# Kernel tuning notes

Hardware: AMD Instinct MI355X
Metric: run time of the kernel (lower is better)

Reference implementation:

```python
import jax, jax.numpy as jnp
import numpy as np

EMBED_DIM = 1024
NUM_HEADS = 16
HEAD_DIM = EMBED_DIM // NUM_HEADS
SCALE = HEAD_DIM ** (-0.5)


def setup_inputs() -> dict:
    key = jax.random.key(0)
    ks = jax.random.split(key, 13)
    B, N, D = 4, 4096, EMBED_DIM
    lin_scale = 1.0 / np.sqrt(D)
    inp = {
        "q": jax.random.normal(ks[0], (B, N, D), dtype=jnp.float32),
        "k": jax.random.normal(ks[1], (B, N, D), dtype=jnp.float32),
        "v": jax.random.normal(ks[2], (B, N, D), dtype=jnp.float32),
        "Wq": jax.random.uniform(ks[3], (D, D), jnp.float32, -lin_scale, lin_scale),
        "bq": jax.random.uniform(ks[4], (D,), jnp.float32, -lin_scale, lin_scale),
        "Wk": jax.random.uniform(ks[5], (D, D), jnp.float32, -lin_scale, lin_scale),
        "bk": jax.random.uniform(ks[6], (D,), jnp.float32, -lin_scale, lin_scale),
        "Wv": jax.random.uniform(ks[7], (D, D), jnp.float32, -lin_scale, lin_scale),
        "bv": jax.random.uniform(ks[8], (D,), jnp.float32, -lin_scale, lin_scale),
        "q_alpha": jax.random.normal(ks[9], (NUM_HEADS, HEAD_DIM), dtype=jnp.float32),
        "k_beta": jax.random.normal(ks[10], (NUM_HEADS, HEAD_DIM), dtype=jnp.float32),
        "Wo": jax.random.uniform(ks[11], (D, D), jnp.float32, -lin_scale, lin_scale),
        "bo": jax.random.uniform(ks[12], (D,), jnp.float32, -lin_scale, lin_scale),
    }
    return inp


def reference(q, k, v, Wq, bq, Wk, bk, Wv, bv, q_alpha, k_beta, Wo, bo):
    B, N, D = q.shape
    H, Dh = NUM_HEADS, HEAD_DIM
    # torch Linear: x @ W.T + b
    Q = (q @ Wq.T + bq).reshape(B, N, H, Dh)
    K = (k @ Wk.T + bk).reshape(B, N, H, Dh)
    V = (v @ Wv.T + bv).reshape(B, N, H, Dh)
    # alpha: [B,N,H] -> softmax over N
    alpha = jnp.einsum('bnhd,hd->bnh', Q, q_alpha) * SCALE
    alpha = jax.nn.softmax(alpha, axis=1)
    # global_q: [B,1,H,Dh]
    global_q = jnp.einsum('bnhd,bnh->bhd', Q, alpha)[:, None]
    P = K * global_q  # [B,N,H,Dh]
    beta = jnp.einsum('bnhd,hd->bnh', P, k_beta) * SCALE
    beta = jax.nn.softmax(beta, axis=1)
    global_v = jnp.einsum('bnhd,bnh->bhd', V, beta)[:, None]
    out = (Q + global_v).reshape(B, N, D)
    out = out @ Wo.T + bo
    return out
```

## Files before the change

### kernel.cpp

```cpp
#include <hip/hip_runtime.h>
#include <hip/hip_bf16.h>
#include <cstdint>
#include <cstddef>

#define SEQ    4096
#define NB     4
#define DIM    1024
#define NHEAD  16
#define HDIM   64
#define MROWS  (NB * SEQ)
#define SCALEF 0.125f
#define NT     16

typedef short          s16x8 __attribute__((ext_vector_type(8)));
typedef unsigned short u16x8 __attribute__((ext_vector_type(8)));
typedef float          f32x4 __attribute__((ext_vector_type(4)));
typedef unsigned short u16;

__device__ __forceinline__ u16 f2bf(float f) {
  return __builtin_bit_cast(u16, __float2bfloat16(f));
}
__device__ __forceinline__ float bf2f(u16 u) {
  return __builtin_bit_cast(float, (uint32_t)u << 16);
}
__device__ __forceinline__ void gload_lds16(const void* g, void* l) {
  __builtin_amdgcn_global_load_lds(
      (const __attribute__((address_space(1))) void*)g,
      (__attribute__((address_space(3))) void*)l, 16, 0, 0);
}

__global__ __launch_bounds__(256) void cvt_weights(
    const float* __restrict__ w0, const float* __restrict__ w1,
    const float* __restrict__ w2, const float* __restrict__ w3,
    u16* __restrict__ o0, u16* __restrict__ o1,
    u16* __restrict__ o2, u16* __restrict__ o3)
{
  int t = blockIdx.x * 256 + threadIdx.x;
  int m = t >> 17;
  int off = (t & 131071) * 8;
  const float* s = (m == 0) ? w0 : (m == 1) ? w1 : (m == 2) ? w2 : w3;
  u16*         d = (m == 0) ? o0 : (m == 1) ? o1 : (m == 2) ? o2 : o3;
  float4 a = ((const float4*)(s + off))[0];
  float4 b = ((const float4*)(s + off))[1];
  u16x8 p;
  p[0] = f2bf(a.x); p[1] = f2bf(a.y); p[2] = f2bf(a.z); p[3] = f2bf(a.w);
  p[4] = f2bf(b.x); p[5] = f2bf(b.y); p[6] = f2bf(b.z); p[7] = f2bf(b.w);
  *(u16x8*)(d + off) = p;
}

__global__ __launch_bounds__(256) void cvt_act(
    const float* __restrict__ s, u16* __restrict__ d)
{
  int t = blockIdx.x * 256 + threadIdx.x;
  int off = t * 8;
  float4 a = ((const float4*)(s + off))[0];
  float4 b = ((const float4*)(s + off))[1];
  u16x8 p;
  p[0] = f2bf(a.x); p[1] = f2bf(a.y); p[2] = f2bf(a.z); p[3] = f2bf(a.w);
  p[4] = f2bf(b.x); p[5] = f2bf(b.y); p[6] = f2bf(b.z); p[7] = f2bf(b.w);
  *(u16x8*)(d + off) = p;
}

template<int MODE>
__global__ __launch_bounds__(512) void gemm256(
    const u16* __restrict__ A, const u16* __restrict__ W,
    const float* __restrict__ bias, u16* __restrict__ Cb, float* __restrict__ Cf,
    const float* __restrict__ c2, int do_alpha,
    const float* __restrict__ qalpha, float* __restrict__ la)
{
  extern __shared__ __align__(16) char smem[];
  const int tid = threadIdx.x;
  const int lane = tid & 63, wave = tid >> 6;
  const int wr = wave >> 2, wc = wave & 3;
  const int fr = lane & 15, fq = lane >> 4;
  const int m0 = blockIdx.x * 256, n0 = blockIdx.y * 256;
  const int wrow = wr * 128, wcol = wc * 64;

  const int arow = tid >> 3;
  const int scol = (((tid & 7) ^ ((tid >> 3) & 7)) * 8);

  f32x4 acc[8][4];
  #pragma unroll
  for (int i = 0; i < 8; ++i)
    #pragma unroll
    for (int j = 0; j < 4; ++j) acc[i][j] = (f32x4){0.f, 0.f, 0.f, 0.f};

  auto stA = [&](int kt, int h) {
    const u16* g = A + (size_t)(m0 + h * 128) * DIM + kt * 64;
    char* l = smem + (kt & 1) * 32768 + h * 16384;
    gload_lds16(g + (size_t)arow * DIM + scol,        l + tid * 16);
    gload_lds16(g + (size_t)(64 + arow) * DIM + scol, l + 8192 + tid * 16);
  };
  auto stB = [&](int kt, int h) {
    const u16* g = W + (size_t)(n0 + h * 128) * DIM + kt * 64;
    char* l = smem + 65536 + (kt & 1) * 32768 + h * 16384;
    gload_lds16(g + (size_t)arow * DIM + scol,        l + tid * 16);
    gload_lds16(g + (size_t)(64 + arow) * DIM + scol, l + 8192 + tid * 16);
  };
  auto ldsoff = [&](int R, int ks) -> size_t {
    return (size_t)R * 128 + (size_t)((ks * 64 + fq * 16) ^ ((R & 7) << 4));
  };

  stA(0, 0); stA(0, 1); stB(0, 0); stB(0, 1);
  stA(1, 0);
  asm volatile("s_waitcnt vmcnt(2)" ::: "memory");
  asm volatile("s_barrier" ::: "memory");

  for (int t = 0; t < NT; ++t) {
    const char* Abase = smem + (t & 1) * 32768;
    const char* Bbase = smem + 65536 + (t & 1) * 32768;
    s16x8 areg[4][2];
    #pragma unroll
    for (int p = 0; p < 4; ++p) {
      const int mq = p >> 1, nq = p & 1;
      s16x8 breg[2][2];
      #pragma unroll
      for (int j = 0; j < 2; ++j)
        #pragma unroll
        for (int ks = 0; ks < 2; ++ks)
          breg[j][ks] = *(const s16x8*)(Bbase + ldsoff(wcol + (nq * 2 + j) * 16 + fr, ks));
      if (nq == 0) {
        #pragma unroll
        for (int i = 0; i < 4; ++i)
          #pragma unroll
          for (int ks = 0; ks < 2; ++ks)
            areg[i][ks] = *(const s16x8*)(Abase + ldsoff(wrow + (mq * 4 + i) * 16 + fr, ks));
      }
      if (p == 0 && t + 1 < NT) stA(t + 1, 1);
      if (p == 1 && t + 1 < NT) stB(t + 1, 0);
      if (p == 2 && t + 1 < NT) stB(t + 1, 1);
      if (p == 3 && t + 2 < NT) stA(t + 2, 0);

      asm volatile("s_barrier" ::: "memory");
      __builtin_amdgcn_s_setprio(1);
      #pragma unroll
      for (int i = 0; i < 4; ++i)
        #pragma unroll
        for (int j = 0; j < 2; ++j)
          #pragma unroll
          for (int ks = 0; ks < 2; ++ks)
            acc[mq * 4 + i][nq * 2 + j] = __builtin_amdgcn_mfma_f32_16x16x32_bf16(
                areg[i][ks], breg[j][ks], acc[mq * 4 + i][nq * 2 + j], 0, 0, 0);
      __builtin_amdgcn_s_setprio(0);
      if (p < 3) {
        asm volatile("s_barrier" ::: "memory");
      } else {
        if (t == NT - 2) asm volatile("s_waitcnt vmcnt(0)" ::: "memory");
        else             asm volatile("s_waitcnt vmcnt(2)" ::: "memory");
        asm volatile("s_barrier" ::: "memory");
      }
    }
  }

  if constexpr (MODE == 0) {
    #pragma unroll
    for (int ni = 0; ni < 4; ++ni) {
      const int col = n0 + wcol + ni * 16 + fr;
      const float bvv = bias[col];
      #pragma unroll
      for (int mi = 0; mi < 8; ++mi)
        #pragma unroll
        for (int r = 0; r < 4; ++r)
          acc[mi][ni][r] += bvv;
    }
    #pragma unroll
    for (int ni = 0; ni < 4; ++ni) {
      const int col = n0 + wcol + ni * 16 + fr;
      #pragma unroll
      for (int mi = 0; mi < 8; ++mi) {
        #pragma unroll
        for (int r = 0; r < 4; ++r) {
          const int row = m0 + wrow + mi * 16 + fq * 4 + r;
          Cb[(size_t)row * DIM + col] = f2bf(acc[mi][ni][r]);
        }
      }
    }
    if (do_alpha) {
      const int h = (n0 >> 6) + wc;
      float qa0 = qalpha[h * HDIM + 0 * 16 + fr];
      float qa1 = qalpha[h * HDIM + 1 * 16 + fr];
      float qa2 = qalpha[h * HDIM + 2 * 16 + fr];
      float qa3 = qalpha[h * HDIM + 3 * 16 + fr];
      #pragma unroll
      for (int mi = 0; mi < 8; ++mi) {
        #pragma unroll
        for (int r = 0; r < 4; ++r) {
          float p = acc[mi][0][r] * qa0 + acc[mi][1][r] * qa1
                  + acc[mi][2][r] * qa2 + acc[mi][3][r] * qa3;
          p += __shfl_xor(p, 1);
          p += __shfl_xor(p, 2);
          p += __shfl_xor(p, 4);
          p += __shfl_xor(p, 8);
          if (fr == 0) {
            const int row = m0 + wrow + mi * 16 + fq * 4 + r;
            la[((size_t)(row >> 12) * NHEAD + h) * SEQ + (row & (SEQ - 1))] = p * SCALEF;
          }
        }
      }
    }
  } else {
    const int bidx = m0 >> 12;
    #pragma unroll
    for (int ni = 0; ni < 4; ++ni) {
      const int col = n0 + wcol + ni * 16 + fr;
      const float cv = c2[bidx * DIM + col];
      #pragma unroll
      for (int mi = 0; mi < 8; ++mi) {
        #pragma unroll
        for (int r = 0; r < 4; ++r) {
          const int row = m0 + wrow + mi * 16 + fq * 4 + r;
          Cf[(size_t)row * DIM + col] = acc[mi][ni][r] + cv;
        }
      }
    }
  }
}

__global__ __launch_bounds__(256) void softmax_norm(
    float* __restrict__ l, float* __restrict__ zbuf)
{
  const int bh = blockIdx.x;
  const int tid = threadIdx.x, lane = tid & 63, wave = tid >> 6;
  float* p = l + (size_t)bh * SEQ;
  __shared__ float red[8];

  float4 v[4];
  #pragma unroll
  for (int i = 0; i < 4; ++i) v[i] = ((const float4*)p)[i * 256 + tid];

  float m = -1e30f;
  #pragma unroll
  for (int i = 0; i < 4; ++i)
    m = fmaxf(m, fmaxf(fmaxf(v[i].x, v[i].y), fmaxf(v[i].z, v[i].w)));
  #pragma unroll
  for (int o = 32; o; o >>= 1) m = fmaxf(m, __shfl_xor(m, o));
  if (lane == 0) red[wave] = m;
  __syncthreads();
  m = fmaxf(fmaxf(red[0], red[1]), fmaxf(red[2], red[3]));

  float s = 0.f;
  #pragma unroll
  for (int i = 0; i < 4; ++i) {
    v[i].x = __expf(v[i].x - m); v[i].y = __expf(v[i].y - m);
    v[i].z = __expf(v[i].z - m); v[i].w = __expf(v[i].w - m);
    s += (v[i].x + v[i].y) + (v[i].z + v[i].w);
  }
  #pragma unroll
  for (int o = 32; o; o >>= 1) s += __shfl_xor(s, o);
  if (lane == 0) red[4 + wave] = s;
  __syncthreads();
  s = (red[4] + red[5]) + (red[6] + red[7]);

  float inv = 1.0f / s;
  #pragma unroll
  for (int i = 0; i < 4; ++i) {
    v[i].x *= inv; v[i].y *= inv; v[i].z *= inv; v[i].w *= inv;
    ((float4*)p)[i * 256 + tid] = v[i];
  }
  if (tid < HDIM) zbuf[bh * HDIM + tid] = 0.f;
}

__global__ __launch_bounds__(256) void accum_weighted(
    const u16* __restrict__ X, const float* __restrict__ w,
    float* __restrict__ outp)
{
  const int bh = blockIdx.y, chunk = blockIdx.x;
  const int b = bh >> 4, h = bh & 15;
  const int tid = threadIdx.x, lane = tid & 63, wave = tid >> 6;
  const int rsub = lane >> 3, cl = lane & 7;
  const size_t base = (size_t)b * SEQ * DIM + h * HDIM;
  const int n0 = chunk * 512;

  float acc[8] = {0, 0, 0, 0, 0, 0, 0, 0};
  for (int it = 0; it < 16; ++it) {
    int n = n0 + it * 32 + wave * 8 + rsub;
    u16x8 u = *(const u16x8*)(X + base + (size_t)n * DIM + cl * 8);
    float wv = w[(size_t)bh * SEQ + n];
    #pragma unroll
    for (int j = 0; j < 8; ++j) acc[j] += wv * bf2f(u[j]);
  }
  #pragma unroll
  for (int j = 0; j < 8; ++j) {
    acc[j] += __shfl_xor(acc[j], 8);
    acc[j] += __shfl_xor(acc[j], 16);
    acc[j] += __shfl_xor(acc[j], 32);
  }
  __shared__ float part[4][64];
  if (rsub == 0) {
    #pragma unroll
    for (int j = 0; j < 8; ++j) part[wave][cl * 8 + j] = acc[j];
  }
  __syncthreads();
  if (tid < HDIM) {
    float s = (part[0][tid] + part[1][tid]) + (part[2][tid] + part[3][tid]);
    atomicAdd(&outp[bh * HDIM + tid], s);
  }
}

__global__ __launch_bounds__(256) void make_vecb(
    const float* __restrict__ gq, const float* __restrict__ kbeta,
    float* __restrict__ vecb)
{
  int t = blockIdx.x * 256 + threadIdx.x;
  int h = (t >> 6) & 15, d = t & 63;
  vecb[t] = gq[t] * kbeta[h * HDIM + d] * SCALEF;
}

__global__ __launch_bounds__(256) void logits_beta(
    const u16* __restrict__ Kb, const float* __restrict__ vecb,
    float* __restrict__ lb)
{
  __shared__ float vb[NHEAD][HDIM];
  const int rg = blockIdx.x;
  const int b = rg >> 8;
  const int tid = threadIdx.x, lane = tid & 63, wave = tid >> 6;

  for (int i = tid; i < NHEAD * HDIM; i += 256)
    ((float*)vb)[i] = vecb[b * DIM + i];
  __syncthreads();

  const int h = lane >> 2, dq = (lane & 3) * 16;
  #pragma unroll
  for (int i = 0; i < 4; ++i) {
    int gr = rg * 16 + wave * 4 + i;
    const u16* rp = Kb + (size_t)gr * DIM + h * HDIM + dq;
    u16x8 u0 = *(const u16x8*)rp;
    u16x8 u1 = *(const u16x8*)(rp + 8);
    float dot = 0.f;
    #pragma unroll
    for (int j = 0; j < 8; ++j) dot += bf2f(u0[j]) * vb[h][dq + j];
    #pragma unroll
    for (int j = 0; j < 8; ++j) dot += bf2f(u1[j]) * vb[h][dq + 8 + j];
    dot += __shfl_xor(dot, 1);
    dot += __shfl_xor(dot, 2);
    if ((lane & 3) == 0) {
      lb[((size_t)b * NHEAD + h) * SEQ + (gr & (SEQ - 1))] = dot;
    }
  }
}

__global__ __launch_bounds__(256) void gv_wo_kernel(
    const float* __restrict__ gv, const float* __restrict__ Wo,
    const float* __restrict__ bo, float* __restrict__ c2)
{
  int wid = blockIdx.x * 4 + (threadIdx.x >> 6);
  int b = wid >> 10, j = wid & 1023;
  int lane = threadIdx.x & 63;
  float acc = 0.f;
  #pragma unroll
  for (int c = 0; c < 16; ++c) {
    int kk = c * 64 + lane;
    acc += gv[b * DIM + kk] * Wo[(size_t)j * DIM + kk];
  }
  #pragma unroll
  for (int o = 32; o; o >>= 1) acc += __shfl_down(acc, o);
  if (lane == 0) c2[wid] = acc + bo[j];
}

extern "C" void kernel_launch(void* const* d_in, const int* in_sizes, int n_in,
                              void* d_out, int out_size, void* d_ws, size_t ws_size,
                              hipStream_t stream) {
  const float* q  = (const float*)d_in[0];
  const float* k  = (const float*)d_in[1];
  const float* v  = (const float*)d_in[2];
  const float* Wq = (const float*)d_in[3];
  const float* bq = (const float*)d_in[4];
  const float* Wk = (const float*)d_in[5];
  const float* bk = (const float*)d_in[6];
  const float* Wv = (const float*)d_in[7];
  const float* bv = (const float*)d_in[8];
  const float* qa = (const float*)d_in[9];
  const float* kb = (const float*)d_in[10];
  const float* Wo = (const float*)d_in[11];
  const float* bo = (const float*)d_in[12];
  float* out = (float*)d_out;

  u16* Qb  = (u16*)d_ws;
  u16* Kb  = Qb + (size_t)MROWS * DIM;
  u16* Vb  = Kb + (size_t)MROWS * DIM;
  u16* Wqb = Vb + (size_t)MROWS * DIM;
  u16* Wkb = Wqb + (size_t)DIM * DIM;
  u16* Wvb = Wkb + (size_t)DIM * DIM;
  u16* Wob = Wvb + (size_t)DIM * DIM;
  float* la   = (float*)(Wob + (size_t)DIM * DIM);
  float* lb   = la + (size_t)NB * NHEAD * SEQ;
  float* gq   = lb + (size_t)NB * NHEAD * SEQ;
  float* gv   = gq + NB * DIM;
  float* vecb = gv + NB * DIM;
  float* c2   = vecb + NB * DIM;

  u16* actb = (u16*)d_out;

  const dim3 g256(MROWS / 256, DIM / 256);
  const size_t ldsb = 131072;

  cvt_weights<<<2048, 256, 0, stream>>>(Wq, Wk, Wv, Wo, Wqb, Wkb, Wvb, Wob);

  cvt_act<<<8192, 256, 0, stream>>>(q, actb);
  gemm256<0><<<g256, 512, ldsb, stream>>>(actb, Wqb, bq, Qb, nullptr, nullptr, 1, qa, la);
  cvt_act<<<8192, 256, 0, stream>>>(k, actb);
  gemm256<0><<<g256, 512, ldsb, stream>>>(actb, Wkb, bk, Kb, nullptr, nullptr, 0, qa, la);
  cvt_act<<<8192, 256, 0, stream>>>(v, actb);
  gemm256<0><<<g256, 512, ldsb, stream>>>(actb, Wvb, bv, Vb, nullptr, nullptr, 0, qa, la);

  softmax_norm<<<64, 256, 0, stream>>>(la, gq);
  accum_weighted<<<dim3(8, 64), 256, 0, stream>>>(Qb, la, gq);
  make_vecb<<<16, 256, 0, stream>>>(gq, kb, vecb);
  logits_beta<<<1024, 256, 0, stream>>>(Kb, vecb, lb);
  softmax_norm<<<64, 256, 0, stream>>>(lb, gv);
  accum_weighted<<<dim3(8, 64), 256, 0, stream>>>(Vb, lb, gv);
  gv_wo_kernel<<<1024, 256, 0, stream>>>(gv, Wo, bo, c2);
  gemm256<1><<<g256, 512, ldsb, stream>>>(Qb, Wob, nullptr, nullptr, out, c2, 0, qa, la);
}
```

Baseline: 251.3 us.

## Overlap activation conversion and reductions with GEMMs via extra producer waves

Adds two extra waves (threads 512-639) to each projection GEMM block. These waves run side work concurrently with the MFMA waves: converting the next activation to bf16, computing the weighted Q accumulation, and computing the beta logits. This removes several separate kernel launches and double-buffers the activation buffer in the output memory. The side waves issue dummy s_barrier instructions to stay matched with the main waves' barriers. The cost is extra register and bandwidth pressure inside the GEMM, and a fragile assumption about how many barriers the main waves execute.

```diff
diff --git a/kernel.cpp b/kernel.cpp
--- a/kernel.cpp
+++ b/kernel.cpp
@@ -62,14 +62,91 @@
 }
 
 template<int MODE>
-__global__ __launch_bounds__(512) void gemm256(
+__global__ __launch_bounds__(640) void gemm256(
     const u16* __restrict__ A, const u16* __restrict__ W,
     const float* __restrict__ bias, u16* __restrict__ Cb, float* __restrict__ Cf,
     const float* __restrict__ c2, int do_alpha,
-    const float* __restrict__ qalpha, float* __restrict__ la)
+    const float* __restrict__ qalpha, float* __restrict__ la,
+    const float* __restrict__ cvt_src, u16* __restrict__ cvt_dst,
+    const u16* __restrict__ ac_X, const float* __restrict__ ac_w,
+    float* __restrict__ ac_out,
+    const u16* __restrict__ lg_K, const float* __restrict__ lg_gq,
+    const float* __restrict__ lg_kbeta, float* __restrict__ lg_out)
 {
   extern __shared__ __align__(16) char smem[];
   const int tid = threadIdx.x;
+  const int gid = blockIdx.x + (blockIdx.y << 6);
+
+  if (tid >= 512) {
+    const int lt = tid - 512;
+    if (cvt_src) {
+      const int xt = (gid << 7) | lt;
+      for (int it = 0; it < 64; ++it) {
+        const size_t off = ((size_t)it * 32768 + xt) * 8;
+        float4 a = ((const float4*)(cvt_src + off))[0];
+        float4 b = ((const float4*)(cvt_src + off))[1];
+        u16x8 p;
+        p[0] = f2bf(a.x); p[1] = f2bf(a.y); p[2] = f2bf(a.z); p[3] = f2bf(a.w);
+        p[4] = f2bf(b.x); p[5] = f2bf(b.y); p[6] = f2bf(b.z); p[7] = f2bf(b.w);
+        *(u16x8*)(cvt_dst + off) = p;
+      }
+    }
+    if (ac_X) {
+      const int bh = gid >> 2, qtr = gid & 3;
+      const int b = bh >> 4, h = bh & 15;
+      const int lane = lt & 63, w2 = lt >> 6;
+      const int rsub = lane >> 3, cl = lane & 7;
+      const size_t base = (size_t)b * SEQ * DIM + h * HDIM;
+      float acc[8] = {0, 0, 0, 0, 0, 0, 0, 0};
+      for (int it = 0; it < 64; ++it) {
+        const int n = qtr * 1024 + it * 16 + w2 * 8 + rsub;
+        u16x8 u = *(const u16x8*)(ac_X + base + (size_t)n * DIM + cl * 8);
+        const float wv = ac_w[(size_t)bh * SEQ + n];
+        #pragma unroll
+        for (int j = 0; j < 8; ++j) acc[j] += wv * bf2f(u[j]);
+      }
+      #pragma unroll
+      for (int j = 0; j < 8; ++j) {
+        acc[j] += __shfl_xor(acc[j], 8);
+        acc[j] += __shfl_xor(acc[j], 16);
+        acc[j] += __shfl_xor(acc[j], 32);
+      }
+      if (rsub == 0) {
+        #pragma unroll
+        for (int j = 0; j < 8; ++j)
+          atomicAdd(&ac_out[bh * HDIM + cl * 8 + j], acc[j]);
+      }
+    }
+    if (lg_K) {
+      const int lane = lt & 63, w2 = lt >> 6;
+      const int gw = gid * 2 + w2;
+      const int h = lane >> 2, dq = (lane & 3) * 16;
+      const int r0 = gw * 32;
+      const int b = r0 >> 12;
+      float vbl[16];
+      #pragma unroll
+      for (int j = 0; j < 16; ++j)
+        vbl[j] = lg_gq[b * DIM + h * HDIM + dq + j] * lg_kbeta[h * HDIM + dq + j] * SCALEF;
+      for (int i = 0; i < 32; ++i) {
+        const int gr = r0 + i;
+        const u16* rp = lg_K + (size_t)gr * DIM + h * HDIM + dq;
+        u16x8 u0 = *(const u16x8*)rp;
+        u16x8 u1 = *(const u16x8*)(rp + 8);
+        float dot = 0.f;
+        #pragma unroll
+        for (int j = 0; j < 8; ++j) dot += bf2f(u0[j]) * vbl[j];
+        #pragma unroll
+        for (int j = 0; j < 8; ++j) dot += bf2f(u1[j]) * vbl[8 + j];
+        dot += __shfl_xor(dot, 1);
+        dot += __shfl_xor(dot, 2);
+        if ((lane & 3) == 0)
+          lg_out[((size_t)b * NHEAD + h) * SEQ + (gr & (SEQ - 1))] = dot;
+      }
+    }
+    for (int i = 0; i < 129; ++i) asm volatile("s_barrier" ::: "memory");
+    return;
+  }
+
   const int lane = tid & 63, wave = tid >> 6;
   const int wr = wave >> 2, wc = wave & 3;
   const int fr = lane & 15, fq = lane >> 4;
@@ -294,48 +371,6 @@
   if (tid < HDIM) {
     float s = (part[0][tid] + part[1][tid]) + (part[2][tid] + part[3][tid]);
     atomicAdd(&outp[bh * HDIM + tid], s);
-  }
-}
-
-__global__ __launch_bounds__(256) void make_vecb(
-    const float* __restrict__ gq, const float* __restrict__ kbeta,
-    float* __restrict__ vecb)
-{
-  int t = blockIdx.x * 256 + threadIdx.x;
-  int h = (t >> 6) & 15, d = t & 63;
-  vecb[t] = gq[t] * kbeta[h * HDIM + d] * SCALEF;
-}
-
-__global__ __launch_bounds__(256) void logits_beta(
-    const u16* __restrict__ Kb, const float* __restrict__ vecb,
-    float* __restrict__ lb)
-{
-  __shared__ float vb[NHEAD][HDIM];
-  const int rg = blockIdx.x;
-  const int b = rg >> 8;
-  const int tid = threadIdx.x, lane = tid & 63, wave = tid >> 6;
-
-  for (int i = tid; i < NHEAD * HDIM; i += 256)
-    ((float*)vb)[i] = vecb[b * DIM + i];
-  __syncthreads();
-
-  const int h = lane >> 2, dq = (lane & 3) * 16;
-  #pragma unroll
-  for (int i = 0; i < 4; ++i) {
-    int gr = rg * 16 + wave * 4 + i;
-    const u16* rp = Kb + (size_t)gr * DIM + h * HDIM + dq;
-    u16x8 u0 = *(const u16x8*)rp;
-    u16x8 u1 = *(const u16x8*)(rp + 8);
-    float dot = 0.f;
-    #pragma unroll
-    for (int j = 0; j < 8; ++j) dot += bf2f(u0[j]) * vb[h][dq + j];
-    #pragma unroll
-    for (int j = 0; j < 8; ++j) dot += bf2f(u1[j]) * vb[h][dq + 8 + j];
-    dot += __shfl_xor(dot, 1);
-    dot += __shfl_xor(dot, 2);
-    if ((lane & 3) == 0) {
-      lb[((size_t)b * NHEAD + h) * SEQ + (gr & (SEQ - 1))] = dot;
-    }
   }
 }
 
@@ -386,29 +421,39 @@
   float* lb   = la + (size_t)NB * NHEAD * SEQ;
   float* gq   = lb + (size_t)NB * NHEAD * SEQ;
   float* gv   = gq + NB * DIM;
-  float* vecb = gv + NB * DIM;
-  float* c2   = vecb + NB * DIM;
-
-  u16* actb = (u16*)d_out;
+  float* c2   = gv + NB * DIM;
+
+  u16* actb0 = (u16*)d_out;
+  u16* actb1 = actb0 + (size_t)MROWS * DIM;
 
   const dim3 g256(MROWS / 256, DIM / 256);
   const size_t ldsb = 131072;
 
   cvt_weights<<<2048, 256, 0, stream>>>(Wq, Wk, Wv, Wo, Wqb, Wkb, Wvb, Wob);
-
-  cvt_act<<<8192, 256, 0, stream>>>(q, actb);
-  gemm256<0><<<g256, 512, ldsb, stream>>>(actb, Wqb, bq, Qb, nullptr, nullptr, 1, qa, la);
-  cvt_act<<<8192, 256, 0, stream>>>(k, actb);
-  gemm256<0><<<g256, 512, ldsb, stream>>>(actb, Wkb, bk, Kb, nullptr, nullptr, 0, qa, la);
-  cvt_act<<<8192, 256, 0, stream>>>(v, actb);
-  gemm256<0><<<g256, 512, ldsb, stream>>>(actb, Wvb, bv, Vb, nullptr, nullptr, 0, qa, la);
-
+  cvt_act<<<8192, 256, 0, stream>>>(q, actb0);
+
+  gemm256<0><<<g256, 640, ldsb, stream>>>(actb0, Wqb, bq, Qb, nullptr, nullptr, 1, qa, la,
+                                          k, actb1,
+                                          nullptr, nullptr, nullptr,
+                                          nullptr, nullptr, nullptr, nullptr);
   softmax_norm<<<64, 256, 0, stream>>>(la, gq);
-  accum_weighted<<<dim3(8, 64), 256, 0, stream>>>(Qb, la, gq);
-  make_vecb<<<16, 256, 0, stream>>>(gq, kb, vecb);
-  logits_beta<<<1024, 256, 0, stream>>>(Kb, vecb, lb);
+
+  gemm256<0><<<g256, 640, ldsb, stream>>>(actb1, Wkb, bk, Kb, nullptr, nullptr, 0, qa, la,
+                                          v, actb0,
+                                          Qb, la, gq,
+                                          nullptr, nullptr, nullptr, nullptr);
+
+  gemm256<0><<<g256, 640, ldsb, stream>>>(actb0, Wvb, bv, Vb, nullptr, nullptr, 0, qa, la,
+                                          nullptr, nullptr,
+                                          nullptr, nullptr, nullptr,
+                                          Kb, gq, kb, lb);
+
   softmax_norm<<<64, 256, 0, stream>>>(lb, gv);
   accum_weighted<<<dim3(8, 64), 256, 0, stream>>>(Vb, lb, gv);
   gv_wo_kernel<<<1024, 256, 0, stream>>>(gv, Wo, bo, c2);
-  gemm256<1><<<g256, 512, ldsb, stream>>>(Qb, Wob, nullptr, nullptr, out, c2, 0, qa, la);
-}
+
+  gemm256<1><<<g256, 512, ldsb, stream>>>(Qb, Wob, nullptr, nullptr, out, c2, 0, qa, la,
+                                          nullptr, nullptr,
+                                          nullptr, nullptr, nullptr,
+                                          nullptr, nullptr, nullptr, nullptr);
+}
```

After: 670.6 us. +166.9%, slower.
